# Performance work log

Hardware: AMD Instinct MI355X
Metric: run time of the kernel (lower is better)

## Reference

```python
import jax, jax.numpy as jnp
import numpy as np

B, S, D, H = 2, 2048, 2048, 16
HD = D // H          # 128, even for RoPE
GS = 0.1             # governance_strength
ROPE_BASE = 10000.0


def _rope_cos_sin(seq_len, dtype):
    # inv_freq over pairs of dims: [HD/2]
    inv_freq = 1.0 / (ROPE_BASE ** (jnp.arange(0, HD, 2, dtype=jnp.float32) / HD))
    t = jnp.arange(seq_len, dtype=jnp.float32)
    freqs = jnp.outer(t, inv_freq)          # [S, HD/2]
    return jnp.cos(freqs).astype(dtype), jnp.sin(freqs).astype(dtype)


def _apply_rope(x, cos, sin):
    # x: [B,H,S,HD]; cos/sin: [S,HD/2] -> broadcast over batch/heads
    x1, x2 = jnp.split(x, 2, axis=-1)
    c = cos[None, None, :, :]
    s = sin[None, None, :, :]
    return jnp.concatenate([x1 * c - x2 * s, x2 * c + x1 * s], axis=-1)


def setup_inputs() -> dict:
    key = jax.random.key(0)
    ks = jax.random.split(key, 8)
    sc = 1.0 / np.sqrt(D)
    return {
        "x": jax.random.normal(ks[0], (B, S, D), jnp.float32),
        "Wq": jax.random.normal(ks[1], (D, D), jnp.float32) * sc,
        "Wk": jax.random.normal(ks[2], (D, D), jnp.float32) * sc,
        "Wv": jax.random.normal(ks[3], (D, D), jnp.float32) * sc,
        "Wo": jax.random.normal(ks[4], (D, D), jnp.float32) * sc,
        "bo": jnp.zeros((D,), jnp.float32),
        "policy_mask": jax.random.uniform(ks[5], (1, H, S, S), jnp.float32),
        "memory_weights": jax.random.uniform(ks[6], (B, 1, 1, S), jnp.float32),
    }


def reference(x, Wq, Wk, Wv, Wo, bo, policy_mask, memory_weights):
    dtype = x.dtype
    scale = HD ** -0.5

    def heads(t):
        return t.reshape(B, S, H, HD).transpose(0, 2, 1, 3)  # [B,H,S,HD]

    q = heads(x @ Wq)
    k = heads(x @ Wk)
    v = heads(x @ Wv)

    cos, sin = _rope_cos_sin(S, dtype)
    q = _apply_rope(q, cos, sin)
    k = _apply_rope(k, cos, sin)

    scores = jnp.einsum("bhqd,bhkd->bhqk", q, k) * scale  # [B,H,S,S]

    # governance bias: policy term + memory-aware log term
    bias = policy_mask * GS + jnp.log1p(memory_weights * GS + 1e-8)
    scores = scores + bias

    # causal mask (no KV cache: kv_len == q_len)
    causal = jnp.tril(jnp.ones((S, S), bool))[None, None]
    scores = jnp.where(causal, scores, jnp.asarray(-1e9, dtype))

    attn = jax.nn.softmax(scores, axis=-1)
    out = jnp.einsum("bhqk,bhkd->bhqd", attn, v)          # [B,H,S,HD]
    out = out.transpose(0, 2, 1, 3).reshape(B, S, D)
    return out @ Wo + bo
```

## Files before the change

kernel.cpp:

```cpp
#include <hip/hip_runtime.h>
#include <hip/hip_bf16.h>
#include <math.h>

#define B_ 2
#define S_ 2048
#define D_ 2048
#define H_ 16
#define HD_ 128
#define NT_ (B_*S_)
#define GS_ 0.1f

typedef _Float16 half8 __attribute__((__vector_size__(16)));
typedef _Float16 half4v __attribute__((__vector_size__(8)));
typedef _Float16 half2v __attribute__((__vector_size__(4)));
typedef float f32x4 __attribute__((__vector_size__(16)));
typedef float f32x16 __attribute__((__vector_size__(64)));

#define VMCNT(n) asm volatile("s_waitcnt vmcnt(" #n ")" ::: "memory")

__device__ __forceinline__ void gload_lds16(const void* g, void* s) {
  __builtin_amdgcn_global_load_lds(
      (const __attribute__((address_space(1))) unsigned int*)g,
      (__attribute__((address_space(3))) unsigned int*)s, 16, 0, 0);
}


__global__ void cvt_f32_to_f16(const float* __restrict__ in, _Float16* __restrict__ out, int n4) {
  int i = blockIdx.x * blockDim.x + threadIdx.x;
  if (i >= n4) return;
  float4 v = ((const float4*)in)[i];
  half4v o = { (_Float16)v.x, (_Float16)v.y, (_Float16)v.z, (_Float16)v.w };
  ((half4v*)out)[i] = o;
}

__global__ void transpose_to_f16(const float* __restrict__ in, _Float16* __restrict__ out, int R, int C) {
  __shared__ float t[32][33];
  int c0 = blockIdx.x*32, r0 = blockIdx.y*32;
  int tx = threadIdx.x, ty = threadIdx.y;
#pragma unroll
  for (int j = 0; j < 32; j += 8)
    t[ty+j][tx] = in[(size_t)(r0+ty+j)*C + c0+tx];
  __syncthreads();
#pragma unroll
  for (int j = 0; j < 32; j += 8)
    out[(size_t)(c0+ty+j)*R + r0+tx] = (_Float16)t[tx][ty+j];
}

__global__ void prep_tables(const float* __restrict__ mw, float* __restrict__ cost,
                            float* __restrict__ sint, float* __restrict__ lmw) {
  int t = blockIdx.x*256 + threadIdx.x;
  if (t < S_*64) {
    int s = t >> 6, d = t & 63;
    float inv = (float)pow(10000.0, -(double)(2*d)/(double)HD_);
    float f = (float)s * inv;
    cost[t] = cosf(f);
    sint[t] = sinf(f);
  }
  if (t < B_*S_) lmw[t] = log1pf(mw[t]*GS_ + 1e-8f);
}


template<bool F32OUT>
__global__ __launch_bounds__(256) void gemm_f16(
    const _Float16* __restrict__ A, const _Float16* __restrict__ Bt,
    void* __restrict__ Cout, const float* __restrict__ bias,
    int M, int N, int K)
{
  __shared__ __align__(16) _Float16 As[128*64];
  __shared__ __align__(16) _Float16 Bs[128*64];
  int n0 = blockIdx.x*128, m0 = blockIdx.y*128;
  int tid = threadIdx.x;
  int w = tid >> 6, l = tid & 63;
  int lhi = l >> 4, llo = l & 15;
  int wr = w >> 1, wc = w & 1;
  const f32x4 fz = {0.f,0.f,0.f,0.f};
  f32x4 acc[4][4];
#pragma unroll
  for (int i = 0; i < 4; ++i)
#pragma unroll
    for (int j = 0; j < 4; ++j) acc[i][j] = fz;

  for (int kt = 0; kt < K; kt += 64) {
#pragma unroll
    for (int i = 0; i < 4; ++i) {
      int sid = i*256 + tid;
      int row = sid >> 3;
      int c   = (sid & 7) ^ (row & 7);
      gload_lds16(A  + (size_t)(m0+row)*K + kt + c*8, (char*)As + (size_t)(i*256 + w*64)*16);
      gload_lds16(Bt + (size_t)(n0+row)*K + kt + c*8, (char*)Bs + (size_t)(i*256 + w*64)*16);
    }
    __syncthreads();
#pragma unroll
    for (int kk = 0; kk < 2; ++kk) {
      half8 a[4], b[4];
#pragma unroll
      for (int mi = 0; mi < 4; ++mi) {
        int row = wr*64 + mi*16 + llo;
        int ch = (kk*4 + lhi) ^ (row & 7);
        a[mi] = *(const half8*)((const char*)As + row*128 + ch*16);
      }
#pragma unroll
      for (int ni = 0; ni < 4; ++ni) {
        int row = wc*64 + ni*16 + llo;
        int ch = (kk*4 + lhi) ^ (row & 7);
        b[ni] = *(const half8*)((const char*)Bs + row*128 + ch*16);
      }
#pragma unroll
      for (int mi = 0; mi < 4; ++mi)
#pragma unroll
        for (int ni = 0; ni < 4; ++ni)
          acc[mi][ni] = __builtin_amdgcn_mfma_f32_16x16x32_f16(a[mi], b[ni], acc[mi][ni], 0, 0, 0);
    }
    __syncthreads();
  }
#pragma unroll
  for (int mi = 0; mi < 4; ++mi)
#pragma unroll
    for (int ni = 0; ni < 4; ++ni)
#pragma unroll
      for (int r = 0; r < 4; ++r) {
        int row = m0 + wr*64 + mi*16 + lhi*4 + r;
        int col = n0 + wc*64 + ni*16 + llo;
        if constexpr (F32OUT)
          ((float*)Cout)[(size_t)row*N + col] = acc[mi][ni][r] + bias[col];
        else
          ((_Float16*)Cout)[(size_t)row*N + col] = (_Float16)acc[mi][ni][r];
      }
}

__global__ void rope_qk(const _Float16* __restrict__ qkv, const float* __restrict__ cost,
                        const float* __restrict__ sint, _Float16* __restrict__ Qr,
                        _Float16* __restrict__ Kr) {
  int token = blockIdx.x;
  int b = token >> 11, s = token & (S_-1);
  int t = threadIdx.x;
  int isk = t >> 7, u = t & 127;
  int hh = u >> 3, dd0 = (u & 7)*8;
  const _Float16* src = qkv + (size_t)token*(3*D_) + (size_t)isk*D_ + hh*128;
  half8 a  = *(const half8*)(src + dd0);
  half8 bb = *(const half8*)(src + 64 + dd0);
  half8 lo, hi;
#pragma unroll
  for (int j = 0; j < 8; ++j) {
    float c  = cost[s*64 + dd0 + j];
    float sn = sint[s*64 + dd0 + j];
    float x1 = (float)a[j], x2 = (float)bb[j];
    lo[j] = (_Float16)(x1*c - x2*sn);
    hi[j] = (_Float16)(x2*c + x1*sn);
  }
  _Float16* dst = (isk ? Kr : Qr) + ((size_t)(b*H_ + hh)*S_ + s)*HD_;
  *(half8*)(dst + dd0) = lo;
  *(half8*)(dst + 64 + dd0) = hi;
}

__global__ void v_transpose(const _Float16* __restrict__ qkv, _Float16* __restrict__ Vt) {
  __shared__ _Float16 tile[64][33];
  int st = blockIdx.x*64;
  int dt = blockIdx.y*32;
  int bh = blockIdx.z;
  int b = bh >> 4, h = bh & 15;
  int t = threadIdx.x;
  int s = t >> 2, dc = (t & 3)*8;
  half8 v = *(const half8*)(qkv + (size_t)(b*S_ + st + s)*(3*D_) + 2*D_ + h*128 + dt + dc);
#pragma unroll
  for (int j = 0; j < 8; ++j) tile[s][dc+j] = v[j];
  __syncthreads();
  int d = t >> 3, sc = (t & 7)*8;
  half8 o;
#pragma unroll
  for (int j = 0; j < 8; ++j) o[j] = tile[sc+j][d];
  *(half8*)(Vt + ((size_t)bh*HD_ + dt + d)*S_ + st + sc) = o;
}

__global__ __launch_bounds__(256) void attn_kernel(
    const _Float16* __restrict__ Qr, const _Float16* __restrict__ Kr,
    const _Float16* __restrict__ Vt, const float* __restrict__ policy,
    const float* __restrict__ lmw, _Float16* __restrict__ Ob)
{
  __shared__ __align__(16) char SMEM[81920];
  int bx = blockIdx.x;
  int qb = (S_/128) - 1 - (bx / (B_*H_));
  int rem = bx % (B_*H_);
  int h = rem >> 1;
  int b = rem & 1;
  int bh = b*H_ + h;
  const _Float16* Qb = Qr + (size_t)bh*S_*HD_;
  const _Float16* Kb = Kr + (size_t)bh*S_*HD_;
  const _Float16* Vb = Vt + (size_t)bh*HD_*S_;
  const float* pol = policy + (size_t)h*S_*S_;
  const float* lmb = lmw + b*S_;
  int tid = threadIdx.x;
  int w = tid >> 6, l = tid & 63;
  int l31 = l & 31, lh = l >> 5;
  int r8 = l >> 3, c8 = l & 7;
  int q0 = qb*128 + w*32;
  int gq = q0 + l31;
  char* Bw = SMEM + 65536 + w*4096;

  auto stageKV = [&](int tt, char* base){
    int kv0s = tt*64;
#pragma unroll
    for (int i = 0; i < 4; ++i) {
      int sid = i*256 + tid;
      int krow = sid >> 4;
      int ck = (sid & 15) ^ (krow & 15);
      gload_lds16(Kb + (size_t)(kv0s+krow)*HD_ + ck*8, base + (size_t)(i*256 + w*64)*16);
      int dv = krow*2 + (ck >> 3);
      gload_lds16(Vb + (size_t)dv*S_ + kv0s + (ck & 7)*8, base + 16384 + (size_t)(i*256 + w*64)*16);
    }
  };

  const float scale = 0.08838834764831845f;
  half8 qf[8];
#pragma unroll
  for (int ds = 0; ds < 8; ++ds) {
    half8 qv = *(const half8*)(Qb + (size_t)gq*HD_ + ds*16 + lh*8);
#pragma unroll
    for (int e = 0; e < 8; ++e) qv[e] = (_Float16)((float)qv[e] * scale);
    qf[ds] = qv;
  }

  f32x16 oacc[4];
#pragma unroll
  for (int i = 0; i < 4; ++i)
#pragma unroll
    for (int r = 0; r < 16; ++r) oacc[i][r] = 0.f;
  float m_ = -INFINITY, l_ = 0.f;

  stageKV(0, SMEM);
  VMCNT(0);
  __builtin_amdgcn_sched_barrier(0);
  __builtin_amdgcn_s_barrier();

  int nt = qb*2 + 2;
  for (int t = 0; t < nt; ++t) {
    int kv0 = t*64;
    char* base = SMEM + (size_t)(t&1)*32768;
    bool pre = (t+1 < nt);

    float4 lmv[2];
    float4 pb[4][2];
#pragma unroll
    for (int ci = 0; ci < 2; ++ci) {
      lmv[ci] = *(const float4*)(lmb + kv0 + ci*32 + c8*4);
#pragma unroll
      for (int ri = 0; ri < 4; ++ri) {
        int qq = q0 + ri*8 + r8;
        pb[ri][ci] = *(const float4*)(pol + (size_t)qq*S_ + kv0 + ci*32 + c8*4);
      }
    }
    __builtin_amdgcn_sched_barrier(0);
    if (pre) stageKV(t+1, SMEM + (size_t)((t+1)&1)*32768);

    f32x16 sacc[2];
#pragma unroll
    for (int kh = 0; kh < 2; ++kh)
#pragma unroll
      for (int r = 0; r < 16; ++r) sacc[kh][r] = 0.f;
    __builtin_amdgcn_s_setprio(1);
#pragma unroll
    for (int kh = 0; kh < 2; ++kh) {
      const char* kbase = base + (kh*32 + l31)*256;
      int sw = l & 15;
#pragma unroll
      for (int ds = 0; ds < 8; ++ds) {
        half8 kf = *(const half8*)(kbase + (((ds*2 + lh) ^ sw) << 4));
        sacc[kh] = __builtin_amdgcn_mfma_f32_32x32x16_f16(kf, qf[ds], sacc[kh], 0, 0, 0);
      }
    }
    __builtin_amdgcn_s_setprio(0);

    if (pre) { VMCNT(8); } else { VMCNT(0); }
    __builtin_amdgcn_sched_barrier(0);
#pragma unroll
    for (int ci = 0; ci < 2; ++ci)
#pragma unroll
      for (int ri = 0; ri < 4; ++ri) {
        int ql = ri*8 + r8;
        float bx_ = fmaf(pb[ri][ci].x, GS_, lmv[ci].x);
        float by_ = fmaf(pb[ri][ci].y, GS_, lmv[ci].y);
        float bz_ = fmaf(pb[ri][ci].z, GS_, lmv[ci].z);
        float bw_ = fmaf(pb[ri][ci].w, GS_, lmv[ci].w);
        half2v h0 = __builtin_amdgcn_cvt_pkrtz(bx_, by_);
        half2v h1 = __builtin_amdgcn_cvt_pkrtz(bz_, bw_);
        half4v o4 = { h0[0], h0[1], h1[0], h1[1] };
        int chunk = (ci*8 + c8) ^ (ql & 15);
        *(half4v*)(Bw + ql*128 + chunk*8) = o4;
      }

    bool domask = (kv0 + 63 > q0);
#pragma unroll
    for (int kh = 0; kh < 2; ++kh)
#pragma unroll
      for (int rq = 0; rq < 4; ++rq) {
        int chunk = 2*rq + lh + 8*kh;
        half4v b4 = *(const half4v*)(Bw + l31*128 + ((chunk ^ (l31 & 15)) << 3));
#pragma unroll
        for (int rm = 0; rm < 4; ++rm) {
          int r = rq*4 + rm;
          float v = sacc[kh][r] + (float)b4[rm];
          int gk = kv0 + kh*32 + rm + 8*rq + 4*lh;
          if (domask && gk > gq) v = -1e9f;
          sacc[kh][r] = v;
        }
      }

    float mx = -INFINITY;
#pragma unroll
    for (int kh = 0; kh < 2; ++kh)
#pragma unroll
      for (int r = 0; r < 16; ++r) mx = fmaxf(mx, sacc[kh][r]);
    mx = fmaxf(mx, __shfl_xor(mx, 32));
    bool skip = __all(mx - m_ <= 8.0f);
    if (!skip) {
      float mnew = fmaxf(m_, mx);
      float fct = __expf(m_ - mnew);
      m_ = mnew;
      l_ *= fct;
#pragma unroll
      for (int i = 0; i < 4; ++i)
#pragma unroll
        for (int r = 0; r < 16; ++r) oacc[i][r] *= fct;
    }
    float rsum = 0.f;
#pragma unroll
    for (int kh = 0; kh < 2; ++kh)
#pragma unroll
      for (int r = 0; r < 16; ++r) {
        float pp = __expf(sacc[kh][r] - m_);
        sacc[kh][r] = pp;
        rsum += pp;
      }
    rsum += __shfl_xor(rsum, 32);
    l_ += rsum;

    half8 pfrag[4];
#pragma unroll
    for (int s = 0; s < 4; ++s) {
      int kh = s >> 1, rb = (s & 1)*8;
      unsigned A0 = __builtin_bit_cast(unsigned, __builtin_amdgcn_cvt_pkrtz(sacc[kh][rb+0], sacc[kh][rb+1]));
      unsigned A1 = __builtin_bit_cast(unsigned, __builtin_amdgcn_cvt_pkrtz(sacc[kh][rb+2], sacc[kh][rb+3]));
      unsigned B0 = __builtin_bit_cast(unsigned, __builtin_amdgcn_cvt_pkrtz(sacc[kh][rb+4], sacc[kh][rb+5]));
      unsigned B1 = __builtin_bit_cast(unsigned, __builtin_amdgcn_cvt_pkrtz(sacc[kh][rb+6], sacc[kh][rb+7]));
      unsigned sA0 = (unsigned)__shfl_xor((int)A0, 32);
      unsigned sA1 = (unsigned)__shfl_xor((int)A1, 32);
      unsigned sB0 = (unsigned)__shfl_xor((int)B0, 32);
      unsigned sB1 = (unsigned)__shfl_xor((int)B1, 32);
      uint4 uu;
      uu.x = lh ? sB0 : A0;
      uu.y = lh ? sB1 : A1;
      uu.z = lh ? B0  : sA0;
      uu.w = lh ? B1  : sA1;
      pfrag[s] = __builtin_bit_cast(half8, uu);
    }

    __builtin_amdgcn_s_setprio(1);
#pragma unroll
    for (int dt = 0; dt < 4; ++dt) {
      int d = dt*32 + l31;
      const char* vbase = base + 16384 + (d >> 1)*256;
      int swv = l31 >> 1;
      int cbase = (d & 1) << 3;
#pragma unroll
      for (int s = 0; s < 4; ++s) {
        half8 vf = *(const half8*)(vbase + (((cbase + s*2 + lh) ^ swv) << 4));
        oacc[dt] = __builtin_amdgcn_mfma_f32_32x32x16_f16(vf, pfrag[s], oacc[dt], 0, 0, 0);
      }
    }
    __builtin_amdgcn_s_setprio(0);

    VMCNT(0);
    __builtin_amdgcn_sched_barrier(0);
    __builtin_amdgcn_s_barrier();
  }

  float inv = 1.f / l_;
  int q = w*32 + l31;
#pragma unroll
  for (int dt = 0; dt < 4; ++dt)
#pragma unroll
    for (int rq = 0; rq < 4; ++rq) {
      half4v o4;
#pragma unroll
      for (int j = 0; j < 4; ++j) o4[j] = (_Float16)(oacc[dt][rq*4+j] * inv);
      int off = q*256 + ((dt*64 + rq*16 + lh*8) ^ ((q & 15) << 4));
      *(half4v*)(SMEM + off) = o4;
    }
  __syncthreads();
  int qr = tid >> 1, hf = tid & 1;
  size_t gbase = ((size_t)(b*S_ + qb*128 + qr))*D_ + h*128 + hf*64;
#pragma unroll
  for (int j = 0; j < 8; ++j) {
    int c = hf*8 + j;
    half8 vv = *(const half8*)(SMEM + qr*256 + ((c ^ (qr & 15)) << 4));
    *(half8*)(Ob + gbase + j*8) = vv;
  }
}


extern "C" void kernel_launch(void* const* d_in, const int* in_sizes, int n_in,
                              void* d_out, int out_size, void* d_ws, size_t ws_size,
                              hipStream_t stream) {
  const float* x   = (const float*)d_in[0];
  const float* Wq  = (const float*)d_in[1];
  const float* Wk  = (const float*)d_in[2];
  const float* Wv  = (const float*)d_in[3];
  const float* Wo  = (const float*)d_in[4];
  const float* bo  = (const float*)d_in[5];
  const float* pol = (const float*)d_in[6];
  const float* mw  = (const float*)d_in[7];
  float* out = (float*)d_out;

  char* p = (char*)d_ws;
  auto take = [&](size_t bytes) { char* r = p; p += (bytes + 255) & ~(size_t)255; return r; };
  _Float16* xb   = (_Float16*)take((size_t)NT_*D_*2);
  _Float16* Wt   = (_Float16*)take((size_t)3*D_*D_*2);
  _Float16* Wot  = (_Float16*)take((size_t)D_*D_*2);
  _Float16* qkv  = (_Float16*)take((size_t)NT_*3*D_*2);
  _Float16* Qr   = (_Float16*)take((size_t)B_*H_*S_*HD_*2);
  _Float16* Kr   = (_Float16*)take((size_t)B_*H_*S_*HD_*2);
  _Float16* Vtb  = (_Float16*)take((size_t)B_*H_*S_*HD_*2);
  _Float16* Ob   = (_Float16*)take((size_t)NT_*D_*2);
  float* cost = (float*)take((size_t)S_*64*4);
  float* sint = (float*)take((size_t)S_*64*4);
  float* lmwb = (float*)take((size_t)B_*S_*4);

  cvt_f32_to_f16<<<(NT_*D_/4 + 255)/256, 256, 0, stream>>>(x, xb, NT_*D_/4);
  transpose_to_f16<<<dim3(64,64), dim3(32,8), 0, stream>>>(Wq, Wt,                    D_, D_);
  transpose_to_f16<<<dim3(64,64), dim3(32,8), 0, stream>>>(Wk, Wt +   (size_t)D_*D_,  D_, D_);
  transpose_to_f16<<<dim3(64,64), dim3(32,8), 0, stream>>>(Wv, Wt + 2*(size_t)D_*D_,  D_, D_);
  transpose_to_f16<<<dim3(64,64), dim3(32,8), 0, stream>>>(Wo, Wot, D_, D_);
  prep_tables<<<512, 256, 0, stream>>>(mw, cost, sint, lmwb);

  gemm_f16<false><<<dim3(3*D_/128, NT_/128), 256, 0, stream>>>(xb, Wt, qkv, nullptr, NT_, 3*D_, D_);
  rope_qk<<<NT_, 256, 0, stream>>>(qkv, cost, sint, Qr, Kr);
  v_transpose<<<dim3(S_/64, HD_/32, B_*H_), 256, 0, stream>>>(qkv, Vtb);
  attn_kernel<<<B_*H_*(S_/128), 256, 0, stream>>>(Qr, Kr, Vtb, pol, lmwb, Ob);
  gemm_f16<true><<<dim3(D_/128, NT_/128), 256, 0, stream>>>(Ob, Wot, out, bo, NT_, D_, D_);
}
```

Before: 355.8 us.

## Restructure attention loop: exp2 softmax, per-wave causal skip, split K/V staging

Folds log2(e) into the Q scale and bias tables so the softmax uses exp2 instead of exp. Warps whose 32-query slice lies entirely before the KV tile skip the bias loads, the MFMAs and the softmax. K is double-buffered and prefetched one tile ahead, while V is single-buffered and loaded during QK^T, which cuts LDS to 64KB and allows more blocks per CU. It also drops launch_bounds and changes the bias LDS swizzle. V now waits with vmcnt(0) inside each iteration, which may expose V load latency.

```diff
diff --git a/kernel.cpp b/kernel.cpp
--- a/kernel.cpp
+++ b/kernel.cpp
@@ -9,6 +9,7 @@
 #define HD_ 128
 #define NT_ (B_*S_)
 #define GS_ 0.1f
+#define LOG2E_ 1.4426950408889634f
 
 typedef _Float16 half8 __attribute__((__vector_size__(16)));
 typedef _Float16 half4v __attribute__((__vector_size__(8)));
@@ -17,6 +18,7 @@
 typedef float f32x16 __attribute__((__vector_size__(64)));
 
 #define VMCNT(n) asm volatile("s_waitcnt vmcnt(" #n ")" ::: "memory")
+#define LGKMCNT0 asm volatile("s_waitcnt lgkmcnt(0)" ::: "memory")
 
 __device__ __forceinline__ void gload_lds16(const void* g, void* s) {
   __builtin_amdgcn_global_load_lds(
@@ -56,7 +58,7 @@
     cost[t] = cosf(f);
     sint[t] = sinf(f);
   }
-  if (t < B_*S_) lmw[t] = log1pf(mw[t]*GS_ + 1e-8f);
+  if (t < B_*S_) lmw[t] = log1pf(mw[t]*GS_ + 1e-8f) * LOG2E_;
 }
 
 
@@ -172,12 +174,12 @@
   *(half8*)(Vt + ((size_t)bh*HD_ + dt + d)*S_ + st + sc) = o;
 }
 
-__global__ __launch_bounds__(256) void attn_kernel(
+__global__ void attn_kernel(
     const _Float16* __restrict__ Qr, const _Float16* __restrict__ Kr,
     const _Float16* __restrict__ Vt, const float* __restrict__ policy,
     const float* __restrict__ lmw, _Float16* __restrict__ Ob)
 {
-  __shared__ __align__(16) char SMEM[81920];
+  __shared__ __align__(16) char SMEM[65536];
   int bx = blockIdx.x;
   int qb = (S_/128) - 1 - (bx / (B_*H_));
   int rem = bx % (B_*H_);
@@ -195,28 +197,39 @@
   int r8 = l >> 3, c8 = l & 7;
   int q0 = qb*128 + w*32;
   int gq = q0 + l31;
-  char* Bw = SMEM + 65536 + w*4096;
-
-  auto stageKV = [&](int tt, char* base){
-    int kv0s = tt*64;
+  char* Bw = SMEM + 49152 + w*4096;
+
+  auto stageK = [&](int tt){
+    char* dstb = SMEM + (size_t)(tt&1)*16384;
+    int kv = tt*64;
 #pragma unroll
     for (int i = 0; i < 4; ++i) {
       int sid = i*256 + tid;
       int krow = sid >> 4;
       int ck = (sid & 15) ^ (krow & 15);
-      gload_lds16(Kb + (size_t)(kv0s+krow)*HD_ + ck*8, base + (size_t)(i*256 + w*64)*16);
+      gload_lds16(Kb + (size_t)(kv+krow)*HD_ + ck*8, dstb + (size_t)(i*256 + w*64)*16);
+    }
+  };
+  auto stageV = [&](int tt){
+    char* dstb = SMEM + 32768;
+    int kv = tt*64;
+#pragma unroll
+    for (int i = 0; i < 4; ++i) {
+      int sid = i*256 + tid;
+      int krow = sid >> 4;
+      int ck = (sid & 15) ^ (krow & 15);
       int dv = krow*2 + (ck >> 3);
-      gload_lds16(Vb + (size_t)dv*S_ + kv0s + (ck & 7)*8, base + 16384 + (size_t)(i*256 + w*64)*16);
+      gload_lds16(Vb + (size_t)dv*S_ + kv + (ck & 7)*8, dstb + (size_t)(i*256 + w*64)*16);
     }
   };
 
-  const float scale = 0.08838834764831845f;
+  const float qscale = 0.08838834764831845f * LOG2E_;
   half8 qf[8];
 #pragma unroll
   for (int ds = 0; ds < 8; ++ds) {
     half8 qv = *(const half8*)(Qb + (size_t)gq*HD_ + ds*16 + lh*8);
 #pragma unroll
-    for (int e = 0; e < 8; ++e) qv[e] = (_Float16)((float)qv[e] * scale);
+    for (int e = 0; e < 8; ++e) qv[e] = (_Float16)((float)qv[e] * qscale);
     qf[ds] = qv;
   }
 
@@ -226,151 +239,157 @@
 #pragma unroll
     for (int r = 0; r < 16; ++r) oacc[i][r] = 0.f;
   float m_ = -INFINITY, l_ = 0.f;
-
-  stageKV(0, SMEM);
+  const float GS2 = GS_ * LOG2E_;
+  int nt = qb*2 + 2;
+
+  stageK(0);
   VMCNT(0);
   __builtin_amdgcn_sched_barrier(0);
   __builtin_amdgcn_s_barrier();
 
-  int nt = qb*2 + 2;
   for (int t = 0; t < nt; ++t) {
     int kv0 = t*64;
-    char* base = SMEM + (size_t)(t&1)*32768;
+    const char* Kbase = SMEM + (size_t)(t&1)*16384;
+    const char* Vbase = SMEM + 32768;
     bool pre = (t+1 < nt);
-
-    float4 lmv[2];
-    float4 pb[4][2];
-#pragma unroll
-    for (int ci = 0; ci < 2; ++ci) {
-      lmv[ci] = *(const float4*)(lmb + kv0 + ci*32 + c8*4);
-#pragma unroll
-      for (int ri = 0; ri < 4; ++ri) {
-        int qq = q0 + ri*8 + r8;
-        pb[ri][ci] = *(const float4*)(pol + (size_t)qq*S_ + kv0 + ci*32 + c8*4);
-      }
-    }
-    __builtin_amdgcn_sched_barrier(0);
-    if (pre) stageKV(t+1, SMEM + (size_t)((t+1)&1)*32768);
+    bool act = (kv0 <= q0 + 31);
+
+    if (pre) stageK(t+1);
+    float4 pb[4][2], lm[2];
+    if (act) {
+#pragma unroll
+      for (int ci = 0; ci < 2; ++ci) {
+        lm[ci] = *(const float4*)(lmb + kv0 + ci*32 + c8*4);
+#pragma unroll
+        for (int ri = 0; ri < 4; ++ri)
+          pb[ri][ci] = *(const float4*)(pol + (size_t)(q0 + ri*8 + r8)*S_ + kv0 + ci*32 + c8*4);
+      }
+    }
+    stageV(t);
 
     f32x16 sacc[2];
-#pragma unroll
-    for (int kh = 0; kh < 2; ++kh)
-#pragma unroll
-      for (int r = 0; r < 16; ++r) sacc[kh][r] = 0.f;
-    __builtin_amdgcn_s_setprio(1);
-#pragma unroll
-    for (int kh = 0; kh < 2; ++kh) {
-      const char* kbase = base + (kh*32 + l31)*256;
-      int sw = l & 15;
-#pragma unroll
-      for (int ds = 0; ds < 8; ++ds) {
-        half8 kf = *(const half8*)(kbase + (((ds*2 + lh) ^ sw) << 4));
-        sacc[kh] = __builtin_amdgcn_mfma_f32_32x32x16_f16(kf, qf[ds], sacc[kh], 0, 0, 0);
-      }
-    }
-    __builtin_amdgcn_s_setprio(0);
-
-    if (pre) { VMCNT(8); } else { VMCNT(0); }
-    __builtin_amdgcn_sched_barrier(0);
-#pragma unroll
-    for (int ci = 0; ci < 2; ++ci)
-#pragma unroll
-      for (int ri = 0; ri < 4; ++ri) {
-        int ql = ri*8 + r8;
-        float bx_ = fmaf(pb[ri][ci].x, GS_, lmv[ci].x);
-        float by_ = fmaf(pb[ri][ci].y, GS_, lmv[ci].y);
-        float bz_ = fmaf(pb[ri][ci].z, GS_, lmv[ci].z);
-        float bw_ = fmaf(pb[ri][ci].w, GS_, lmv[ci].w);
-        half2v h0 = __builtin_amdgcn_cvt_pkrtz(bx_, by_);
-        half2v h1 = __builtin_amdgcn_cvt_pkrtz(bz_, bw_);
-        half4v o4 = { h0[0], h0[1], h1[0], h1[1] };
-        int chunk = (ci*8 + c8) ^ (ql & 15);
-        *(half4v*)(Bw + ql*128 + chunk*8) = o4;
-      }
-
-    bool domask = (kv0 + 63 > q0);
-#pragma unroll
-    for (int kh = 0; kh < 2; ++kh)
-#pragma unroll
-      for (int rq = 0; rq < 4; ++rq) {
-        int chunk = 2*rq + lh + 8*kh;
-        half4v b4 = *(const half4v*)(Bw + l31*128 + ((chunk ^ (l31 & 15)) << 3));
-#pragma unroll
-        for (int rm = 0; rm < 4; ++rm) {
-          int r = rq*4 + rm;
-          float v = sacc[kh][r] + (float)b4[rm];
-          int gk = kv0 + kh*32 + rm + 8*rq + 4*lh;
-          if (domask && gk > gq) v = -1e9f;
-          sacc[kh][r] = v;
+    if (act) {
+#pragma unroll
+      for (int kh = 0; kh < 2; ++kh)
+#pragma unroll
+        for (int r = 0; r < 16; ++r) sacc[kh][r] = 0.f;
+      __builtin_amdgcn_s_setprio(1);
+#pragma unroll
+      for (int kh = 0; kh < 2; ++kh) {
+        const char* kbase = Kbase + (kh*32 + l31)*256;
+        int sw = l31 & 15;
+#pragma unroll
+        for (int ds = 0; ds < 8; ++ds) {
+          half8 kf = *(const half8*)(kbase + (((ds*2 + lh) ^ sw) << 4));
+          sacc[kh] = __builtin_amdgcn_mfma_f32_32x32x16_f16(kf, qf[ds], sacc[kh], 0, 0, 0);
         }
       }
-
-    float mx = -INFINITY;
-#pragma unroll
-    for (int kh = 0; kh < 2; ++kh)
-#pragma unroll
-      for (int r = 0; r < 16; ++r) mx = fmaxf(mx, sacc[kh][r]);
-    mx = fmaxf(mx, __shfl_xor(mx, 32));
-    bool skip = __all(mx - m_ <= 8.0f);
-    if (!skip) {
-      float mnew = fmaxf(m_, mx);
-      float fct = __expf(m_ - mnew);
-      m_ = mnew;
-      l_ *= fct;
-#pragma unroll
-      for (int i = 0; i < 4; ++i)
-#pragma unroll
-        for (int r = 0; r < 16; ++r) oacc[i][r] *= fct;
-    }
-    float rsum = 0.f;
-#pragma unroll
-    for (int kh = 0; kh < 2; ++kh)
-#pragma unroll
-      for (int r = 0; r < 16; ++r) {
-        float pp = __expf(sacc[kh][r] - m_);
-        sacc[kh][r] = pp;
-        rsum += pp;
-      }
-    rsum += __shfl_xor(rsum, 32);
-    l_ += rsum;
-
-    half8 pfrag[4];
-#pragma unroll
-    for (int s = 0; s < 4; ++s) {
-      int kh = s >> 1, rb = (s & 1)*8;
-      unsigned A0 = __builtin_bit_cast(unsigned, __builtin_amdgcn_cvt_pkrtz(sacc[kh][rb+0], sacc[kh][rb+1]));
-      unsigned A1 = __builtin_bit_cast(unsigned, __builtin_amdgcn_cvt_pkrtz(sacc[kh][rb+2], sacc[kh][rb+3]));
-      unsigned B0 = __builtin_bit_cast(unsigned, __builtin_amdgcn_cvt_pkrtz(sacc[kh][rb+4], sacc[kh][rb+5]));
-      unsigned B1 = __builtin_bit_cast(unsigned, __builtin_amdgcn_cvt_pkrtz(sacc[kh][rb+6], sacc[kh][rb+7]));
-      unsigned sA0 = (unsigned)__shfl_xor((int)A0, 32);
-      unsigned sA1 = (unsigned)__shfl_xor((int)A1, 32);
-      unsigned sB0 = (unsigned)__shfl_xor((int)B0, 32);
-      unsigned sB1 = (unsigned)__shfl_xor((int)B1, 32);
-      uint4 uu;
-      uu.x = lh ? sB0 : A0;
-      uu.y = lh ? sB1 : A1;
-      uu.z = lh ? B0  : sA0;
-      uu.w = lh ? B1  : sA1;
-      pfrag[s] = __builtin_bit_cast(half8, uu);
-    }
-
-    __builtin_amdgcn_s_setprio(1);
-#pragma unroll
-    for (int dt = 0; dt < 4; ++dt) {
-      int d = dt*32 + l31;
-      const char* vbase = base + 16384 + (d >> 1)*256;
-      int swv = l31 >> 1;
-      int cbase = (d & 1) << 3;
-#pragma unroll
-      for (int s = 0; s < 4; ++s) {
-        half8 vf = *(const half8*)(vbase + (((cbase + s*2 + lh) ^ swv) << 4));
-        oacc[dt] = __builtin_amdgcn_mfma_f32_32x32x16_f16(vf, pfrag[s], oacc[dt], 0, 0, 0);
-      }
-    }
-    __builtin_amdgcn_s_setprio(0);
+      __builtin_amdgcn_s_setprio(0);
+    }
 
     VMCNT(0);
     __builtin_amdgcn_sched_barrier(0);
+
+    if (act) {
+#pragma unroll
+      for (int ci = 0; ci < 2; ++ci)
+#pragma unroll
+        for (int ri = 0; ri < 4; ++ri) {
+          float bx_ = fmaf(pb[ri][ci].x, GS2, lm[ci].x);
+          float by_ = fmaf(pb[ri][ci].y, GS2, lm[ci].y);
+          float bz_ = fmaf(pb[ri][ci].z, GS2, lm[ci].z);
+          float bw_ = fmaf(pb[ri][ci].w, GS2, lm[ci].w);
+          half2v h0 = __builtin_amdgcn_cvt_pkrtz(bx_, by_);
+          half2v h1 = __builtin_amdgcn_cvt_pkrtz(bz_, bw_);
+          half4v o4 = { h0[0], h0[1], h1[0], h1[1] };
+          int g = ci*8 + c8;
+          *(half4v*)(Bw + g*256 + (((ri*8 + r8) ^ (2*g)) & 31)*8) = o4;
+        }
+      LGKMCNT0;
+      __builtin_amdgcn_sched_barrier(0);
+
+      bool domask = (kv0 + 63 > q0);
+#pragma unroll
+      for (int kh = 0; kh < 2; ++kh)
+#pragma unroll
+        for (int rq = 0; rq < 4; ++rq) {
+          int g = kh*8 + 2*rq + lh;
+          half4v b4 = *(const half4v*)(Bw + g*256 + (((l31 ^ (2*g)) & 31)*8));
+#pragma unroll
+          for (int rm = 0; rm < 4; ++rm) {
+            int r = rq*4 + rm;
+            float v = sacc[kh][r] + (float)b4[rm];
+            int gk = kv0 + kh*32 + rm + 8*rq + 4*lh;
+            if (domask && gk > gq) v = -1e9f;
+            sacc[kh][r] = v;
+          }
+        }
+
+      float mx = -INFINITY;
+#pragma unroll
+      for (int kh = 0; kh < 2; ++kh)
+#pragma unroll
+        for (int r = 0; r < 16; ++r) mx = fmaxf(mx, sacc[kh][r]);
+      mx = fmaxf(mx, __shfl_xor(mx, 32));
+      bool skip = __all(mx - m_ <= 11.5f);
+      if (!skip) {
+        float mnew = fmaxf(m_, mx);
+        float fct = exp2f(m_ - mnew);
+        m_ = mnew;
+        l_ *= fct;
+#pragma unroll
+        for (int i = 0; i < 4; ++i)
+#pragma unroll
+          for (int r = 0; r < 16; ++r) oacc[i][r] *= fct;
+      }
+      float rsum = 0.f;
+#pragma unroll
+      for (int kh = 0; kh < 2; ++kh)
+#pragma unroll
+        for (int r = 0; r < 16; ++r) {
+          float pp = exp2f(sacc[kh][r] - m_);
+          sacc[kh][r] = pp;
+          rsum += pp;
+        }
+      rsum += __shfl_xor(rsum, 32);
+      l_ += rsum;
+
+      half8 pfrag[4];
+#pragma unroll
+      for (int s = 0; s < 4; ++s) {
+        int kh = s >> 1, rb = (s & 1)*8;
+        unsigned A0 = __builtin_bit_cast(unsigned, __builtin_amdgcn_cvt_pkrtz(sacc[kh][rb+0], sacc[kh][rb+1]));
+        unsigned A1 = __builtin_bit_cast(unsigned, __builtin_amdgcn_cvt_pkrtz(sacc[kh][rb+2], sacc[kh][rb+3]));
+        unsigned B0 = __builtin_bit_cast(unsigned, __builtin_amdgcn_cvt_pkrtz(sacc[kh][rb+4], sacc[kh][rb+5]));
+        unsigned B1 = __builtin_bit_cast(unsigned, __builtin_amdgcn_cvt_pkrtz(sacc[kh][rb+6], sacc[kh][rb+7]));
+        unsigned sA0 = (unsigned)__shfl_xor((int)A0, 32);
+        unsigned sA1 = (unsigned)__shfl_xor((int)A1, 32);
+        unsigned sB0 = (unsigned)__shfl_xor((int)B0, 32);
+        unsigned sB1 = (unsigned)__shfl_xor((int)B1, 32);
+        uint4 uu;
+        uu.x = lh ? sB0 : A0;
+        uu.y = lh ? sB1 : A1;
+        uu.z = lh ? B0  : sA0;
+        uu.w = lh ? B1  : sA1;
+        pfrag[s] = __builtin_bit_cast(half8, uu);
+      }
+
+      __builtin_amdgcn_s_setprio(1);
+#pragma unroll
+      for (int dt = 0; dt < 4; ++dt) {
+        int d = dt*32 + l31;
+        const char* vbase = Vbase + (d >> 1)*256;
+        int swv = l31 >> 1;
+        int cbase = (d & 1) << 3;
+#pragma unroll
+        for (int s = 0; s < 4; ++s) {
+          half8 vf = *(const half8*)(vbase + (((cbase + s*2 + lh) ^ swv) << 4));
+          oacc[dt] = __builtin_amdgcn_mfma_f32_32x32x16_f16(vf, pfrag[s], oacc[dt], 0, 0, 0);
+        }
+      }
+      __builtin_amdgcn_s_setprio(0);
+    }
+
     __builtin_amdgcn_s_barrier();
   }
 
```

After: 964.5 us. 2.71x slower.
